# Kernel optimization log

Hardware: AMD Instinct MI355X
Metric: run time of the kernel (lower is better)

## Reference

```python
import jax, jax.numpy as jnp
import numpy as np

SEQ_LEN = 1024
D_MODEL = 512
K_FILT = 24
HEADS = 8
R = 512  # must equal d_model for the module's forward to type-check
NFFT = 2048  # nearest power of two >= 2*SEQ_LEN-1
LN_EPS = 1e-5


def _spectral_filters():
    # Hankel matrix Z[i,j] = 2 / ((i+j)^3 - (i+j)), i,j in 1..T
    e = np.arange(1, SEQ_LEN + 1, dtype=np.float64)
    ipj = e[:, None] + e[None, :]
    Z = 2.0 / (ipj ** 3 - ipj)
    sigma, phi = np.linalg.eigh(Z)
    sigma_k = np.clip(sigma[-K_FILT:], 1e-9, None)
    phi_k = phi[:, -K_FILT:] * sigma_k ** 0.25
    return phi_k.astype(np.float32)  # (T, K)


def setup_inputs() -> dict:
    key = jax.random.key(0)
    ks = jax.random.split(key, 12)
    s = 0.02
    B = 2

    def lin(k):
        kw, kb = jax.random.split(k)
        return (jax.random.normal(kw, (D_MODEL, D_MODEL), jnp.float32) * s,
                jax.random.normal(kb, (D_MODEL,), jnp.float32) * s)

    Wq, bq = lin(ks[0]); Wk, bk = lin(ks[1]); Wv, bv = lin(ks[2])
    Wg, bg = lin(ks[3]); Wo, bo = lin(ks[4])
    return {
        'x': jax.random.normal(ks[5], (B, SEQ_LEN, D_MODEL), jnp.float32),
        'stu_filters': jnp.asarray(_spectral_filters()),
        'M_inputs': jax.random.normal(ks[6], (D_MODEL, R), jnp.float32) * s,
        'M_filters': jax.random.normal(ks[7], (K_FILT, R), jnp.float32) * s,
        'Wq': Wq, 'bq': bq, 'Wk': Wk, 'bk': bk, 'Wv': Wv, 'bv': bv,
        'Wg': Wg, 'bg': bg, 'Wo': Wo, 'bo': bo,
        'ln_w': jnp.ones((R,), jnp.float32),
        'ln_b': jnp.zeros((R,), jnp.float32),
    }


def _stu_conv(u, v):
    # u: (B, T, r), v: (T, r). FFT-based causal conv with sign featurization.
    T = u.shape[1]
    sgn = jnp.where(jnp.arange(T) % 2 == 1, -1.0, 1.0)[None, :, None]  # (1,T,1)
    Vf = jnp.fft.rfft(v[None, :, :, None], n=NFFT, axis=1)  # (1,F,r,1)
    U = jnp.stack([u, u * sgn], axis=-1)  # (B,T,r,2)
    Uf = jnp.fft.rfft(U, n=NFFT, axis=1)  # (B,F,r,2)
    conv = jnp.fft.irfft(Vf * Uf, n=NFFT, axis=1)[:, :T]  # (B,T,r,2)
    return conv[..., 0], conv[..., 1] * sgn


def _layernorm(x, w, b):
    mu = jnp.mean(x, axis=-1, keepdims=True)
    var = jnp.mean((x - mu) ** 2, axis=-1, keepdims=True)
    return (x - mu) * jax.lax.rsqrt(var + LN_EPS) * w + b


def reference(x, stu_filters, M_inputs, M_filters, Wq, bq, Wk, bk, Wv, bv,
              Wg, bg, Wo, bo, ln_w, ln_b):
    B, T, d = x.shape
    hd = d // HEADS
    # STU features
    u_proj = x @ M_inputs                    # (B,T,r)
    phi_proj = stu_filters @ M_filters       # (T,r)
    sp, sm = _stu_conv(u_proj, phi_proj)
    x_tilde = _layernorm(sp + sm, ln_w, ln_b)  # (B,T,r==d)
    # gated linear attention with gelu features and causal cumsum state
    def proj(W, b):
        y = (x @ W.T + b).reshape(B, T, HEADS, hd).transpose(0, 2, 1, 3)
        return jax.nn.gelu(y, approximate=True)
    Q = proj(Wq, bq); K = proj(Wk, bk); V = proj(Wv, bv)
    Zt = jnp.einsum('bhtp,bhtn->bhtpn', V, K)   # (B,H,T,hd,hd)
    Hc = jnp.cumsum(Zt, axis=2)
    Y = jnp.einsum('bhtp,bhtpn->bhtn', Q, Hc)   # (B,H,T,hd)
    Y_attn = Y.transpose(0, 2, 1, 3).reshape(B, T, d)
    gate = jax.nn.sigmoid(x @ Wg.T + bg)
    comb = gate * Y_attn + (1.0 - gate) * x_tilde
    return comb @ Wo.T + bo
```

## Files before the change

kernel.cpp:

```cpp
#include <hip/hip_runtime.h>
#include <hip/hip_bf16.h>

#define T_SEQ 1024
#define D_MOD 512
#define NHEAD 8
#define HDIM  64
#define R_DIM 512
#define BATCH 2

typedef __attribute__((ext_vector_type(8))) __bf16 bf16x8;
typedef __attribute__((ext_vector_type(4))) __bf16 bf16x4;
typedef __attribute__((ext_vector_type(4))) float f32x4;

__device__ __forceinline__ float ldin(const void* p, size_t i, int bf) {
    if (bf) return __bfloat162float(((const __hip_bfloat16*)p)[i]);
    return ((const float*)p)[i];
}
__device__ __forceinline__ void stout(void* p, size_t i, int bf, float v) {
    if (bf) ((__hip_bfloat16*)p)[i] = __float2bfloat16(v);
    else    ((float*)p)[i] = v;
}

__device__ __forceinline__ float gelu_f(float x) {
    return 0.5f * x * (1.f + tanhf(0.7978845608028654f * (x + 0.044715f * x * x * x)));
}

__device__ __forceinline__ bf16x8 cvt8(float4 a, float4 b) {
    bf16x8 t;
    t[0]=(__bf16)a.x; t[1]=(__bf16)a.y; t[2]=(__bf16)a.z; t[3]=(__bf16)a.w;
    t[4]=(__bf16)b.x; t[5]=(__bf16)b.y; t[6]=(__bf16)b.z; t[7]=(__bf16)b.w;
    return t;
}

__device__ __forceinline__ int detect_bf(const void* x) {
    __shared__ int cnt;
    if (threadIdx.x == 0) cnt = 0;
    __syncthreads();
    const unsigned short* h = (const unsigned short*)x;
    int c = 0;
    for (int i = threadIdx.x; i < 8192; i += 256)
        if ((h[i] & 0x7F80u) == 0x7F80u) c++;
    if (c) atomicAdd(&cnt, c);
    __syncthreads();
    return cnt == 0;
}

__global__ __launch_bounds__(256) void mega_gemm(
    const void* __restrict__ x, const void* __restrict__ Mi,
    const void* __restrict__ stf, const void* __restrict__ Mf,
    const void* __restrict__ Wq, const void* __restrict__ bq,
    const void* __restrict__ Wk, const void* __restrict__ bk,
    const void* __restrict__ Wv, const void* __restrict__ bv,
    const void* __restrict__ Wg, const void* __restrict__ bg,
    __bf16* __restrict__ fu, __bf16* __restrict__ fphi,
    __bf16* __restrict__ fQ, __bf16* __restrict__ fKT,
    __bf16* __restrict__ fV, __bf16* __restrict__ fG)
{
    const int tid = threadIdx.x;
    const int job = blockIdx.z;
    if (job == 6) {
        float4* zp = (float4*)(fphi + 524288);
        const int bid = blockIdx.y * 8 + blockIdx.x;
        const float4 z4 = make_float4(0.f, 0.f, 0.f, 0.f);
        #pragma unroll
        for (int q = 0; q < 8; ++q)
            zp[(size_t)bid * 2048 + q * 256 + tid] = z4;
        return;
    }
    const int bf = detect_bf(x);
    const void* A = x; const void* Bw; const void* bias = nullptr;
    int Kd = 512, act = 0; bool trb = true;
    switch (job) {
        case 0: Bw = Mi; trb = false; break;
        case 1: Bw = Wq; bias = bq; act = 1; break;
        case 2: Bw = Wk; bias = bk; act = 1; break;
        case 3: Bw = Wv; bias = bv; act = 1; break;
        case 4: Bw = Wg; bias = bg; act = 2; break;
        default: A = stf; Bw = Mf; trb = false; Kd = 32; break;
    }
    const int M = (job == 5) ? 1024 : 2048;
    const int m0 = blockIdx.y * 64;
    if (m0 >= M) return;
    const int n0 = blockIdx.x * 64;

    __shared__ __align__(16) __bf16 As[64][40];
    __shared__ __align__(16) __bf16 Bs[64][40];
    const int wave = tid >> 6, lane = tid & 63;
    const int lm = lane & 15, kq = lane >> 4;

    f32x4 acc[4] = {};

    for (int k0 = 0; k0 < Kd; k0 += 32) {
        if (k0) __syncthreads();
        {
            const int mo = tid >> 2;
            const int ko = (tid & 3) * 8;
            if (job == 5) {
                #pragma unroll
                for (int q = 0; q < 8; ++q) {
                    const int k = ko + q;
                    As[mo][k] = (k < 24) ? (__bf16)ldin(A, (size_t)(m0 + mo) * 24 + k, bf)
                                         : (__bf16)0.f;
                }
            } else if (bf) {
                *(bf16x8*)&As[mo][ko] =
                    *(const bf16x8*)((const __bf16*)A + (size_t)(m0 + mo) * 512 + k0 + ko);
            } else {
                const float* Af = (const float*)A + (size_t)(m0 + mo) * 512 + k0 + ko;
                *(bf16x8*)&As[mo][ko] = cvt8(*(const float4*)Af, *(const float4*)(Af + 4));
            }
        }
        if (trb) {
            const int no = tid >> 2;
            const int ko = (tid & 3) * 8;
            const size_t go = (size_t)(n0 + no) * 512 + k0 + ko;
            if (bf) {
                *(bf16x8*)&Bs[no][ko] = *(const bf16x8*)((const __bf16*)Bw + go);
            } else {
                const float* Bf = (const float*)Bw + go;
                *(bf16x8*)&Bs[no][ko] = cvt8(*(const float4*)Bf, *(const float4*)(Bf + 4));
            }
        } else {
            const int kk = tid >> 3;
            const int nn = (tid & 7) * 8;
            if (job == 5) {
                #pragma unroll
                for (int q = 0; q < 8; ++q)
                    Bs[nn + q][kk] = (kk < 24) ? (__bf16)ldin(Bw, (size_t)kk * 512 + n0 + nn + q, bf)
                                               : (__bf16)0.f;
            } else {
                const size_t off = (size_t)(k0 + kk) * 512 + n0 + nn;
                if (bf) {
                    const bf16x8 t = *(const bf16x8*)((const __bf16*)Bw + off);
                    #pragma unroll
                    for (int q = 0; q < 8; ++q) Bs[nn + q][kk] = t[q];
                } else {
                    const float* Bf = (const float*)Bw + off;
                    #pragma unroll
                    for (int q = 0; q < 8; ++q) Bs[nn + q][kk] = (__bf16)Bf[q];
                }
            }
        }
        __syncthreads();
        const bf16x8 a = *(const bf16x8*)&As[wave * 16 + lm][kq * 8];
        #pragma unroll
        for (int nt = 0; nt < 4; ++nt) {
            const bf16x8 b = *(const bf16x8*)&Bs[nt * 16 + lm][kq * 8];
            acc[nt] = __builtin_amdgcn_mfma_f32_16x16x32_bf16(a, b, acc[nt], 0, 0, 0);
        }
    }
    #pragma unroll
    for (int nt = 0; nt < 4; ++nt) {
        const int n = n0 + nt * 16 + lm;
        #pragma unroll
        for (int r2 = 0; r2 < 4; ++r2) {
            const int m = m0 + wave * 16 + kq * 4 + r2;
            float v = acc[nt][r2];
            if (bias) v += ldin(bias, (size_t)n, bf);
            if (act == 1) v = gelu_f(v);
            if (act == 2) v = 1.f / (1.f + expf(-v));
            switch (job) {
                case 0: fu[(size_t)m * 512 + n] = (__bf16)v; break;
                case 5: fphi[(size_t)m * 512 + n] = (__bf16)v; break;
                case 1: fQ[(size_t)m * 512 + n] = (__bf16)v; break;
                case 3: fV[(size_t)m * 512 + n] = (__bf16)v; break;
                case 4: fG[(size_t)m * 512 + n] = (__bf16)v; break;
                case 2: {
                    const int b = m >> 10, t = m & 1023;
                    const int h = n >> 6,  p = n & 63;
                    fKT[(((size_t)b * NHEAD + h) * 64 + p) * T_SEQ + t] = (__bf16)v;
                    break;
                }
            }
        }
    }
}

__global__ __launch_bounds__(256) void conv_attn_k(
    const __bf16* __restrict__ u, const __bf16* __restrict__ vphi,
    float* __restrict__ w,
    const __bf16* __restrict__ Q, const __bf16* __restrict__ KT,
    const __bf16* __restrict__ V, float* __restrict__ Y)
{
    __shared__ __align__(16) unsigned char smem[49152];
    const int tid = threadIdx.x;
    const int z = blockIdx.z;
    int rem = blockIdx.x, ti = 0;
    while (rem >= ((ti + 4) >> 2)) { rem -= (ti + 4) >> 2; ++ti; }
    const int jlo = rem * 4;
    const int jhi = (jlo + 3 < ti) ? jlo + 3 : ti;
    const int t0 = ti * 64;

    if (z < 2) {
        float (*vs)[64] = (float (*)[64])smem;
        float (*us)[64] = (float (*)[64])(smem + 16384);
        const int rl = tid & 63, tg = tid >> 6;
        const int b = z;
        const int r0 = blockIdx.y * 64;
        const __bf16* ub = u + (size_t)b * T_SEQ * R_DIM;
        float acc[16] = {};
        for (int j = jlo; j <= jhi; ++j) {
            if (j != jlo) __syncthreads();
            const int L0 = j * 64;
            const int W0 = t0 - L0 - 63;
            #pragma unroll
            for (int jj = 0; jj < 8; ++jj) {
                const int n = jj * 256 + tid;
                const int row = n >> 4, c4 = (n & 15) * 4;
                int s = W0 + row;
                s = s < 0 ? 0 : (s > T_SEQ - 1 ? T_SEQ - 1 : s);
                const bf16x4 t = *(const bf16x4*)&ub[(size_t)s * R_DIM + r0 + c4];
                *(float4*)&us[row][c4] =
                    make_float4((float)t[0], (float)t[1], (float)t[2], (float)t[3]);
            }
            #pragma unroll
            for (int jj = 0; jj < 4; ++jj) {
                const int n = jj * 256 + tid;
                const int row = n >> 4, c4 = (n & 15) * 4;
                const bf16x4 t = *(const bf16x4*)&vphi[(size_t)(L0 + row) * R_DIM + r0 + c4];
                *(float4*)&vs[row][c4] =
                    make_float4((float)t[0], (float)t[1], (float)t[2], (float)t[3]);
            }
            __syncthreads();
            if (j < ti) {
                #pragma unroll
                for (int g = 0; g < 4; ++g) {
                    const int wsmin = tg * 16 + 49 - 16 * g;
                    float ur[30];
                    #pragma unroll
                    for (int q = 0; q < 30; ++q) ur[q] = us[wsmin + q][rl];
                    float vr[8];
                    #pragma unroll
                    for (int e = 0; e < 8; ++e) vr[e] = vs[16 * g + 2 * e][rl];
                    #pragma unroll
                    for (int e = 0; e < 8; ++e)
                        #pragma unroll
                        for (int i = 0; i < 16; ++i)
                            acc[i] += vr[e] * ur[i - 2 * e + 14];
                }
            } else {
                for (int l = 0; l < 64; l += 2) {
                    const float vv = vs[l][rl];
                    #pragma unroll
                    for (int i = 0; i < 16; ++i) {
                        const int srel = tg * 16 + i - l;
                        if (srel >= 0) acc[i] += vv * us[srel + 63][rl];
                    }
                }
            }
        }
        #pragma unroll
        for (int i = 0; i < 16; ++i)
            atomicAdd(&w[((size_t)b * T_SEQ + t0 + tg * 16 + i) * R_DIM + r0 + rl],
                      2.f * acc[i]);
    } else {
        __bf16 (*Qs)[72] = (__bf16 (*)[72])smem;
        __bf16 (*Vs)[72] = (__bf16 (*)[72])(smem + 9216);
        __bf16 (*Kt)[72] = (__bf16 (*)[72])(smem + 18432);
        __bf16 (*Sa)[72] = (__bf16 (*)[72])(smem + 27648);
        const int wave = tid >> 6, lane = tid & 63;
        const int lm = lane & 15, kq = lane >> 4;
        const int b = z - 2;
        const int h = blockIdx.y;
        const size_t cbase = ((size_t)b * T_SEQ) * D_MOD + h * HDIM;
        const __bf16* KTh = KT + (((size_t)b * NHEAD + h) * 64) * T_SEQ;
        #pragma unroll
        for (int it = 0; it < 2; ++it) {
            const int n = it * 256 + tid;
            const int row = n >> 3, p0 = (n & 7) * 8;
            *(bf16x8*)&Qs[row][p0] = *(const bf16x8*)&Q[cbase + (size_t)(t0 + row) * D_MOD + p0];
        }
        f32x4 accY[4] = {};
        for (int j = jlo; j <= jhi; ++j) {
            const int s0 = j * 64;
            __syncthreads();
            #pragma unroll
            for (int it = 0; it < 2; ++it) {
                const int n = it * 256 + tid;
                const int row = n >> 3, c0 = (n & 7) * 8;
                *(bf16x8*)&Vs[row][c0] = *(const bf16x8*)&V[cbase + (size_t)(s0 + row) * D_MOD + c0];
                *(bf16x8*)&Kt[row][c0] = *(const bf16x8*)&KTh[(size_t)row * T_SEQ + s0 + c0];
            }
            __syncthreads();
            f32x4 sacc[4] = {};
            #pragma unroll
            for (int ks = 0; ks < 2; ++ks) {
                const bf16x8 a = *(const bf16x8*)&Qs[wave * 16 + lm][ks * 32 + kq * 8];
                #pragma unroll
                for (int nt = 0; nt < 4; ++nt) {
                    const bf16x8 bb = *(const bf16x8*)&Vs[nt * 16 + lm][ks * 32 + kq * 8];
                    sacc[nt] = __builtin_amdgcn_mfma_f32_16x16x32_bf16(a, bb, sacc[nt], 0, 0, 0);
                }
            }
            const bool diag = (j == ti);
            #pragma unroll
            for (int nt = 0; nt < 4; ++nt) {
                const int sl = nt * 16 + lm;
                #pragma unroll
                for (int r2 = 0; r2 < 4; ++r2) {
                    const int tl = wave * 16 + kq * 4 + r2;
                    float v = sacc[nt][r2];
                    if (diag && sl > tl) v = 0.f;
                    Sa[tl][sl] = (__bf16)v;
                }
            }
            #pragma unroll
            for (int ks = 0; ks < 2; ++ks) {
                const bf16x8 a = *(const bf16x8*)&Sa[wave * 16 + lm][ks * 32 + kq * 8];
                #pragma unroll
                for (int nt = 0; nt < 4; ++nt) {
                    const bf16x8 bb = *(const bf16x8*)&Kt[nt * 16 + lm][ks * 32 + kq * 8];
                    accY[nt] = __builtin_amdgcn_mfma_f32_16x16x32_bf16(a, bb, accY[nt], 0, 0, 0);
                }
            }
        }
        #pragma unroll
        for (int nt = 0; nt < 4; ++nt) {
            const int nh = nt * 16 + lm;
            #pragma unroll
            for (int r2 = 0; r2 < 4; ++r2) {
                const int tl = wave * 16 + kq * 4 + r2;
                atomicAdd(&Y[cbase + (size_t)(t0 + tl) * D_MOD + nh], accY[nt][r2]);
            }
        }
    }
}

__global__ __launch_bounds__(256) void ln_k(const float* __restrict__ w,
                                            __bf16* __restrict__ xt,
                                            const void* __restrict__ g,
                                            const void* __restrict__ b,
                                            const void* __restrict__ xref)
{
    const int bf = detect_bf(xref);
    const size_t row = (size_t)blockIdx.y * T_SEQ + blockIdx.x;
    const float* p = w + row * R_DIM;
    const int tid = threadIdx.x;
    const float x0 = p[tid], x1 = p[tid + 256];
    __shared__ float red[4];
    float s = x0 + x1;
    #pragma unroll
    for (int off = 32; off > 0; off >>= 1) s += __shfl_down(s, off, 64);
    if ((tid & 63) == 0) red[tid >> 6] = s;
    __syncthreads();
    const float mu = (red[0] + red[1] + red[2] + red[3]) * (1.f / 512.f);
    __syncthreads();
    const float d0 = x0 - mu, d1 = x1 - mu;
    float vsum = d0 * d0 + d1 * d1;
    #pragma unroll
    for (int off = 32; off > 0; off >>= 1) vsum += __shfl_down(vsum, off, 64);
    if ((tid & 63) == 0) red[tid >> 6] = vsum;
    __syncthreads();
    const float var = (red[0] + red[1] + red[2] + red[3]) * (1.f / 512.f);
    const float rs = rsqrtf(var + 1e-5f);
    __bf16* q = xt + row * R_DIM;
    q[tid]       = (__bf16)(d0 * rs * ldin(g, tid, bf)       + ldin(b, tid, bf));
    q[tid + 256] = (__bf16)(d1 * rs * ldin(g, tid + 256, bf) + ldin(b, tid + 256, bf));
}

__global__ __launch_bounds__(256) void final_gemm(const __bf16* __restrict__ G,
                                                  const float* __restrict__ Yf,
                                                  const __bf16* __restrict__ Xt,
                                                  const void* __restrict__ Wo,
                                                  const void* __restrict__ bo,
                                                  void* __restrict__ out,
                                                  const void* __restrict__ xref)
{
    const int bf = detect_bf(xref);
    __shared__ __align__(16) __bf16 sm[2][2 * 64 * 40];
    const int tid = threadIdx.x;
    const int wave = tid >> 6, lane = tid & 63;
    const int lm = lane & 15, kq = lane >> 4;
    const int mo = tid >> 2, ko = (tid & 3) * 8;
    const int m0 = blockIdx.y * 64, n0 = blockIdx.x * 64;

    bf16x8 pg, px, pw;
    float4 py0, py1, pw0, pw1;

    auto issue = [&](int k0) {
        const size_t off = (size_t)(m0 + mo) * 512 + k0 + ko;
        pg  = *(const bf16x8*)(G + off);
        px  = *(const bf16x8*)(Xt + off);
        py0 = *(const float4*)(Yf + off); py1 = *(const float4*)(Yf + off + 4);
        const size_t ob = (size_t)(n0 + mo) * 512 + k0 + ko;
        if (bf) pw = *(const bf16x8*)((const __bf16*)Wo + ob);
        else { const float* Bf = (const float*)Wo + ob;
               pw0 = *(const float4*)Bf; pw1 = *(const float4*)(Bf + 4); }
    };
    auto commit = [&](int bi) {
        __bf16 (*As)[40] = (__bf16 (*)[40])sm[bi];
        __bf16 (*Bs)[40] = (__bf16 (*)[40])(sm[bi] + 64 * 40);
        const float yv[8] = {py0.x,py0.y,py0.z,py0.w,py1.x,py1.y,py1.z,py1.w};
        bf16x8 t;
        #pragma unroll
        for (int q = 0; q < 8; ++q) {
            const float gg = (float)pg[q];
            t[q] = (__bf16)(gg * yv[q] + (1.f - gg) * (float)px[q]);
        }
        *(bf16x8*)&As[mo][ko] = t;
        *(bf16x8*)&Bs[mo][ko] = bf ? pw : cvt8(pw0, pw1);
    };

    f32x4 acc[4] = {};
    issue(0);
    commit(0);
    __syncthreads();
    int cur = 0;
    for (int k0 = 0; k0 < 512; k0 += 32) {
        const bool haveNext = (k0 + 32 < 512);
        if (haveNext) issue(k0 + 32);
        __bf16 (*As)[40] = (__bf16 (*)[40])sm[cur];
        __bf16 (*Bs)[40] = (__bf16 (*)[40])(sm[cur] + 64 * 40);
        const bf16x8 a = *(const bf16x8*)&As[wave * 16 + lm][kq * 8];
        #pragma unroll
        for (int nt = 0; nt < 4; ++nt) {
            const bf16x8 b = *(const bf16x8*)&Bs[nt * 16 + lm][kq * 8];
            acc[nt] = __builtin_amdgcn_mfma_f32_16x16x32_bf16(a, b, acc[nt], 0, 0, 0);
        }
        if (haveNext) {
            commit(cur ^ 1);
            __syncthreads();
            cur ^= 1;
        }
    }
    #pragma unroll
    for (int nt = 0; nt < 4; ++nt) {
        const int n = n0 + nt * 16 + lm;
        #pragma unroll
        for (int r2 = 0; r2 < 4; ++r2) {
            const int m = m0 + wave * 16 + kq * 4 + r2;
            float v = acc[nt][r2] + ldin(bo, (size_t)n, bf);
            stout(out, (size_t)m * 512 + n, bf, v);
        }
    }
}

extern "C" void kernel_launch(void* const* d_in, const int* in_sizes, int n_in,
                              void* d_out, int out_size, void* d_ws, size_t ws_size,
                              hipStream_t stream)
{
    const void* x   = d_in[0];
    const void* stf = d_in[1];
    const void* Mi  = d_in[2];
    const void* Mf  = d_in[3];
    const void* Wq  = d_in[4];  const void* bq = d_in[5];
    const void* Wk  = d_in[6];  const void* bk = d_in[7];
    const void* Wv  = d_in[8];  const void* bv = d_in[9];
    const void* Wg  = d_in[10]; const void* bg = d_in[11];
    const void* Wo  = d_in[12]; const void* bo = d_in[13];
    const void* lnw = d_in[14]; const void* lnb = d_in[15];

    float* base = (float*)d_ws;
    __bf16* f_u   = (__bf16*)base;
    __bf16* f_phi = f_u + 1048576;
    float*  f_w   = base + 786432;
    float*  f_Y   = base + 1835008;
    __bf16* f_xt  = (__bf16*)(base + 2883584);
    __bf16* f_Q   = (__bf16*)(base + 3407872);
    __bf16* f_KT  = f_Q + 1048576;
    __bf16* f_V   = f_KT + 1048576;
    __bf16* f_G   = f_V + 1048576;

    dim3 blk(256);

    mega_gemm<<<dim3(8, 32, 7), blk, 0, stream>>>(
        x, Mi, stf, Mf, Wq, bq, Wk, bk, Wv, bv, Wg, bg,
        f_u, f_phi, f_Q, f_KT, f_V, f_G);

    conv_attn_k<<<dim3(40, 8, 4), blk, 0, stream>>>(f_u, f_phi, f_w, f_Q, f_KT, f_V, f_Y);

    ln_k<<<dim3(T_SEQ, BATCH), blk, 0, stream>>>(f_w, f_xt, lnw, lnb, x);

    final_gemm<<<dim3(8, 32), blk, 0, stream>>>(f_G, f_Y, f_xt, Wo, bo, d_out, x);
}
```

Measured before the change: 183.8 us.

## Halve final GEMM M-tile to double block count and drop double buffering

The output GEMM now uses 32x64 tiles instead of 64x64, so it launches twice as many blocks (512 instead of 256) to fill more of the GPU's compute units. The register-prefetch double-buffered pipeline is replaced by a simple load, sync, compute loop with a single shared buffer. Each wave now computes a 16x32 sub-tile. The risks are exposed global-load latency without prefetch, and the Wo tile plus the gate/combine arithmetic being redone by twice as many blocks.

```diff
diff --git a/kernel.cpp b/kernel.cpp
--- a/kernel.cpp
+++ b/kernel.cpp
@@ -367,68 +367,60 @@
                                                   const void* __restrict__ xref)
 {
     const int bf = detect_bf(xref);
-    __shared__ __align__(16) __bf16 sm[2][2 * 64 * 40];
+    __shared__ __align__(16) __bf16 As[32][40];
+    __shared__ __align__(16) __bf16 Bs[64][40];
     const int tid = threadIdx.x;
     const int wave = tid >> 6, lane = tid & 63;
     const int lm = lane & 15, kq = lane >> 4;
-    const int mo = tid >> 2, ko = (tid & 3) * 8;
-    const int m0 = blockIdx.y * 64, n0 = blockIdx.x * 64;
-
-    bf16x8 pg, px, pw;
-    float4 py0, py1, pw0, pw1;
-
-    auto issue = [&](int k0) {
-        const size_t off = (size_t)(m0 + mo) * 512 + k0 + ko;
-        pg  = *(const bf16x8*)(G + off);
-        px  = *(const bf16x8*)(Xt + off);
-        py0 = *(const float4*)(Yf + off); py1 = *(const float4*)(Yf + off + 4);
-        const size_t ob = (size_t)(n0 + mo) * 512 + k0 + ko;
-        if (bf) pw = *(const bf16x8*)((const __bf16*)Wo + ob);
-        else { const float* Bf = (const float*)Wo + ob;
-               pw0 = *(const float4*)Bf; pw1 = *(const float4*)(Bf + 4); }
-    };
-    auto commit = [&](int bi) {
-        __bf16 (*As)[40] = (__bf16 (*)[40])sm[bi];
-        __bf16 (*Bs)[40] = (__bf16 (*)[40])(sm[bi] + 64 * 40);
-        const float yv[8] = {py0.x,py0.y,py0.z,py0.w,py1.x,py1.y,py1.z,py1.w};
-        bf16x8 t;
-        #pragma unroll
-        for (int q = 0; q < 8; ++q) {
-            const float gg = (float)pg[q];
-            t[q] = (__bf16)(gg * yv[q] + (1.f - gg) * (float)px[q]);
-        }
-        *(bf16x8*)&As[mo][ko] = t;
-        *(bf16x8*)&Bs[mo][ko] = bf ? pw : cvt8(pw0, pw1);
-    };
-
-    f32x4 acc[4] = {};
-    issue(0);
-    commit(0);
-    __syncthreads();
-    int cur = 0;
+    const int m0 = blockIdx.y * 32, n0 = blockIdx.x * 64;
+    const int mw = (wave & 1) * 16, nw = (wave >> 1) * 32;
+
+    f32x4 acc[2] = {};
+
     for (int k0 = 0; k0 < 512; k0 += 32) {
-        const bool haveNext = (k0 + 32 < 512);
-        if (haveNext) issue(k0 + 32);
-        __bf16 (*As)[40] = (__bf16 (*)[40])sm[cur];
-        __bf16 (*Bs)[40] = (__bf16 (*)[40])(sm[cur] + 64 * 40);
-        const bf16x8 a = *(const bf16x8*)&As[wave * 16 + lm][kq * 8];
-        #pragma unroll
-        for (int nt = 0; nt < 4; ++nt) {
-            const bf16x8 b = *(const bf16x8*)&Bs[nt * 16 + lm][kq * 8];
+        if (k0) __syncthreads();
+        if (tid < 128) {
+            const int mo = tid >> 2;
+            const int ko = (tid & 3) * 8;
+            const size_t off = (size_t)(m0 + mo) * 512 + k0 + ko;
+            const bf16x8 g8 = *(const bf16x8*)(G + off);
+            const bf16x8 x8 = *(const bf16x8*)(Xt + off);
+            const float4 y0 = *(const float4*)(Yf + off);
+            const float4 y1 = *(const float4*)(Yf + off + 4);
+            const float yv[8] = {y0.x,y0.y,y0.z,y0.w,y1.x,y1.y,y1.z,y1.w};
+            bf16x8 t;
+            #pragma unroll
+            for (int q = 0; q < 8; ++q) {
+                const float gg = (float)g8[q];
+                t[q] = (__bf16)(gg * yv[q] + (1.f - gg) * (float)x8[q]);
+            }
+            *(bf16x8*)&As[mo][ko] = t;
+        }
+        {
+            const int no = tid >> 2;
+            const int ko = (tid & 3) * 8;
+            const size_t ob = (size_t)(n0 + no) * 512 + k0 + ko;
+            if (bf) {
+                *(bf16x8*)&Bs[no][ko] = *(const bf16x8*)((const __bf16*)Wo + ob);
+            } else {
+                const float* Bf = (const float*)Wo + ob;
+                *(bf16x8*)&Bs[no][ko] = cvt8(*(const float4*)Bf, *(const float4*)(Bf + 4));
+            }
+        }
+        __syncthreads();
+        const bf16x8 a = *(const bf16x8*)&As[mw + lm][kq * 8];
+        #pragma unroll
+        for (int nt = 0; nt < 2; ++nt) {
+            const bf16x8 b = *(const bf16x8*)&Bs[nw + nt * 16 + lm][kq * 8];
             acc[nt] = __builtin_amdgcn_mfma_f32_16x16x32_bf16(a, b, acc[nt], 0, 0, 0);
         }
-        if (haveNext) {
-            commit(cur ^ 1);
-            __syncthreads();
-            cur ^= 1;
-        }
     }
     #pragma unroll
-    for (int nt = 0; nt < 4; ++nt) {
-        const int n = n0 + nt * 16 + lm;
+    for (int nt = 0; nt < 2; ++nt) {
+        const int n = n0 + nw + nt * 16 + lm;
         #pragma unroll
         for (int r2 = 0; r2 < 4; ++r2) {
-            const int m = m0 + wave * 16 + kq * 4 + r2;
+            const int m = m0 + mw + kq * 4 + r2;
             float v = acc[nt][r2] + ldin(bo, (size_t)n, bf);
             stout(out, (size_t)m * 512 + n, bf, v);
         }
@@ -471,5 +463,5 @@
 
     ln_k<<<dim3(T_SEQ, BATCH), blk, 0, stream>>>(f_w, f_xt, lnw, lnb, x);
 
-    final_gemm<<<dim3(8, 32), blk, 0, stream>>>(f_G, f_Y, f_xt, Wo, bo, d_out, x);
-}
+    final_gemm<<<dim3(8, 64), blk, 0, stream>>>(f_G, f_Y, f_xt, Wo, bo, d_out, x);
+}
```

Result: slower. 188.4 us (+2.5%).

## Fuse LayerNorm into conv kernel via last-block-done atomic counter

Applied to the files above, without the earlier changes.

Removes the separate LayerNorm kernel launch. Each conv block increments a per-(batch, time-tile) counter after its atomic accumulation, and the last block to finish a tile normalizes those 64 rows and writes the bf16 output. The counters are zeroed in the first GEMM kernel. This saves a launch and a full pass over the intermediate. In exchange it adds a fence and a counter atomic to every conv block, leaves the LN work on a few straggler blocks, and switches to a one-pass variance formula.

```diff
diff --git a/kernel.cpp b/kernel.cpp
--- a/kernel.cpp
+++ b/kernel.cpp
@@ -54,7 +54,8 @@
     const void* __restrict__ Wg, const void* __restrict__ bg,
     __bf16* __restrict__ fu, __bf16* __restrict__ fphi,
     __bf16* __restrict__ fQ, __bf16* __restrict__ fKT,
-    __bf16* __restrict__ fV, __bf16* __restrict__ fG)
+    __bf16* __restrict__ fV, __bf16* __restrict__ fG,
+    int* __restrict__ cnt)
 {
     const int tid = threadIdx.x;
     const int job = blockIdx.z;
@@ -65,6 +66,7 @@
         #pragma unroll
         for (int q = 0; q < 8; ++q)
             zp[(size_t)bid * 2048 + q * 256 + tid] = z4;
+        if (bid == 0 && tid < 32) cnt[tid] = 0;
         return;
     }
     const int bf = detect_bf(x);
@@ -178,11 +180,15 @@
 
 __global__ __launch_bounds__(256) void conv_attn_k(
     const __bf16* __restrict__ u, const __bf16* __restrict__ vphi,
-    float* __restrict__ w,
+    float* __restrict__ w, __bf16* __restrict__ xt,
     const __bf16* __restrict__ Q, const __bf16* __restrict__ KT,
-    const __bf16* __restrict__ V, float* __restrict__ Y)
+    const __bf16* __restrict__ V, float* __restrict__ Y,
+    const void* __restrict__ lnw, const void* __restrict__ lnb,
+    int* __restrict__ cnt, const void* __restrict__ xref)
 {
     __shared__ __align__(16) unsigned char smem[49152];
+    __shared__ int lastLN;
+    const int bf = detect_bf(xref);
     const int tid = threadIdx.x;
     const int z = blockIdx.z;
     int rem = blockIdx.x, ti = 0;
@@ -253,6 +259,48 @@
         for (int i = 0; i < 16; ++i)
             atomicAdd(&w[((size_t)b * T_SEQ + t0 + tg * 16 + i) * R_DIM + r0 + rl],
                       2.f * acc[i]);
+
+        __threadfence();
+        __syncthreads();
+        if (tid == 0) {
+            const int expected = 8 * ((ti + 4) >> 2);
+            lastLN = (atomicAdd(&cnt[b * 16 + ti], 1) == expected - 1);
+        }
+        __syncthreads();
+        if (lastLN) {
+            __threadfence();
+            const int wave = tid >> 6, lane = tid & 63;
+            float ga[8], be[8];
+            #pragma unroll
+            for (int q = 0; q < 8; ++q) {
+                ga[q] = ldin(lnw, (size_t)(lane * 8 + q), bf);
+                be[q] = ldin(lnb, (size_t)(lane * 8 + q), bf);
+            }
+            for (int r = 0; r < 16; ++r) {
+                const size_t row = (size_t)b * T_SEQ + t0 + wave * 16 + r;
+                const float* p = w + row * R_DIM + lane * 8;
+                const float4 v0 = *(const float4*)p;
+                const float4 v1 = *(const float4*)(p + 4);
+                const float xv[8] = {v0.x,v0.y,v0.z,v0.w,v1.x,v1.y,v1.z,v1.w};
+                float s = 0.f, ss = 0.f;
+                #pragma unroll
+                for (int q = 0; q < 8; ++q) { s += xv[q]; ss += xv[q] * xv[q]; }
+                #pragma unroll
+                for (int off = 32; off > 0; off >>= 1) {
+                    s  += __shfl_down(s, off, 64);
+                    ss += __shfl_down(ss, off, 64);
+                }
+                s = __shfl(s, 0, 64); ss = __shfl(ss, 0, 64);
+                const float mu = s * (1.f / 512.f);
+                const float var = ss * (1.f / 512.f) - mu * mu;
+                const float rs = rsqrtf(var + 1e-5f);
+                bf16x8 t;
+                #pragma unroll
+                for (int q = 0; q < 8; ++q)
+                    t[q] = (__bf16)((xv[q] - mu) * rs * ga[q] + be[q]);
+                *(bf16x8*)&xt[row * R_DIM + lane * 8] = t;
+            }
+        }
     } else {
         __bf16 (*Qs)[72] = (__bf16 (*)[72])smem;
         __bf16 (*Vs)[72] = (__bf16 (*)[72])(smem + 9216);
@@ -324,38 +372,6 @@
             }
         }
     }
-}
-
-__global__ __launch_bounds__(256) void ln_k(const float* __restrict__ w,
-                                            __bf16* __restrict__ xt,
-                                            const void* __restrict__ g,
-                                            const void* __restrict__ b,
-                                            const void* __restrict__ xref)
-{
-    const int bf = detect_bf(xref);
-    const size_t row = (size_t)blockIdx.y * T_SEQ + blockIdx.x;
-    const float* p = w + row * R_DIM;
-    const int tid = threadIdx.x;
-    const float x0 = p[tid], x1 = p[tid + 256];
-    __shared__ float red[4];
-    float s = x0 + x1;
-    #pragma unroll
-    for (int off = 32; off > 0; off >>= 1) s += __shfl_down(s, off, 64);
-    if ((tid & 63) == 0) red[tid >> 6] = s;
-    __syncthreads();
-    const float mu = (red[0] + red[1] + red[2] + red[3]) * (1.f / 512.f);
-    __syncthreads();
-    const float d0 = x0 - mu, d1 = x1 - mu;
-    float vsum = d0 * d0 + d1 * d1;
-    #pragma unroll
-    for (int off = 32; off > 0; off >>= 1) vsum += __shfl_down(vsum, off, 64);
-    if ((tid & 63) == 0) red[tid >> 6] = vsum;
-    __syncthreads();
-    const float var = (red[0] + red[1] + red[2] + red[3]) * (1.f / 512.f);
-    const float rs = rsqrtf(var + 1e-5f);
-    __bf16* q = xt + row * R_DIM;
-    q[tid]       = (__bf16)(d0 * rs * ldin(g, tid, bf)       + ldin(b, tid, bf));
-    q[tid + 256] = (__bf16)(d1 * rs * ldin(g, tid + 256, bf) + ldin(b, tid + 256, bf));
 }
 
 __global__ __launch_bounds__(256) void final_gemm(const __bf16* __restrict__ G,
@@ -455,8 +471,9 @@
     __bf16* f_phi = f_u + 1048576;
     float*  f_w   = base + 786432;
     float*  f_Y   = base + 1835008;
-    __bf16* f_xt  = (__bf16*)(base + 2883584);
-    __bf16* f_Q   = (__bf16*)(base + 3407872);
+    int*    f_cnt = (int*)(base + 2883584);
+    __bf16* f_xt  = (__bf16*)(base + 2883648);
+    __bf16* f_Q   = (__bf16*)(base + 3407936);
     __bf16* f_KT  = f_Q + 1048576;
     __bf16* f_V   = f_KT + 1048576;
     __bf16* f_G   = f_V + 1048576;
@@ -465,11 +482,10 @@
 
     mega_gemm<<<dim3(8, 32, 7), blk, 0, stream>>>(
         x, Mi, stf, Mf, Wq, bq, Wk, bk, Wv, bv, Wg, bg,
-        f_u, f_phi, f_Q, f_KT, f_V, f_G);
-
-    conv_attn_k<<<dim3(40, 8, 4), blk, 0, stream>>>(f_u, f_phi, f_w, f_Q, f_KT, f_V, f_Y);
-
-    ln_k<<<dim3(T_SEQ, BATCH), blk, 0, stream>>>(f_w, f_xt, lnw, lnb, x);
+        f_u, f_phi, f_Q, f_KT, f_V, f_G, f_cnt);
+
+    conv_attn_k<<<dim3(40, 8, 4), blk, 0, stream>>>(
+        f_u, f_phi, f_w, f_xt, f_Q, f_KT, f_V, f_Y, lnw, lnb, f_cnt, x);
 
     final_gemm<<<dim3(8, 32), blk, 0, stream>>>(f_G, f_Y, f_xt, Wo, bo, d_out, x);
 }
```

Measured after the change: 228.2 us. 1.24x slower.
